# Kernel optimization log

Hardware: AMD Instinct MI355X
Metric: run time of the kernel (lower is better)

Reference implementation:

```python
import jax, jax.numpy as jnp
import numpy as np

B, N, H, A = 8, 2048, 512, 128


def setup_inputs() -> dict:
    key = jax.random.key(0)
    ks = jax.random.split(key, 7)
    s_h = 1.0 / np.sqrt(H)
    s_a = 1.0 / np.sqrt(A)
    return {
        "x": jax.random.normal(ks[0], (B, N, H), dtype=jnp.float32),
        "Wq": jax.random.uniform(ks[1], (H, A), jnp.float32, -s_h, s_h),
        "bq": jax.random.uniform(ks[2], (A,), jnp.float32, -s_h, s_h),
        "Wk": jax.random.uniform(ks[3], (H, A), jnp.float32, -s_h, s_h),
        "bk": jax.random.uniform(ks[4], (A,), jnp.float32, -s_h, s_h),
        "Wv": jax.random.uniform(ks[5], (A, 1), jnp.float32, -s_a, s_a),
        "bv": jax.random.uniform(ks[6], (1,), jnp.float32, -s_a, s_a),
    }


def reference(x, Wq, bq, Wk, bk, Wv, bv):
    # x: [B, N, H]
    Qw = x @ Wq + bq              # [B, N, A]
    Kw = x @ Wk + bk              # [B, N, A]
    g = jax.nn.sigmoid((Qw @ Wv + bv)[..., 0])  # [B, N] per-token gate

    n = x.shape[1]
    scores = jnp.einsum("bnd,bmd->bnm", Qw, Kw)  # [B, N, N]
    diag = jnp.eye(n, dtype=bool)
    # M adds -inf on the diagonal (ones + -inf = -inf), 0 elsewhere
    scores = jnp.where(diag, -jnp.inf, scores)
    P = jax.nn.softmax(scores, axis=-1)          # diagonal prob is exactly 0

    # D + (I - D) @ P with D = diag_embed(g) reduces to a per-row scale:
    # row i -> (1 - g_i) * P[i, :] plus g_i on the diagonal (P[i,i] == 0).
    eye = jnp.eye(n, dtype=P.dtype)
    out = (1.0 - g)[..., None] * P + eye * g[..., None]
    return out
```

## Files before the change

kernel.cpp:

```cpp
#include <hip/hip_runtime.h>
#include <hip/hip_bf16.h>
#include <math.h>

constexpr int B = 8, N = 2048, H = 512, A = 128;

typedef _Float16 f16x8 __attribute__((ext_vector_type(8)));
typedef float f32x4 __attribute__((ext_vector_type(4)));
typedef unsigned short ushort_t;
typedef unsigned int uint_t;

__device__ __forceinline__ f32x4 mfma16h(f16x8 a, f16x8 b, f32x4 c) {
    return __builtin_amdgcn_mfma_f32_16x16x32_f16(a, b, c, 0, 0, 0);
}
__device__ __forceinline__ ushort_t f2h(float v) {
    return __builtin_bit_cast(ushort_t, (_Float16)v);
}
__device__ __forceinline__ float h2f(ushort_t u) {
    return (float)__builtin_bit_cast(_Float16, u);
}
__device__ __forceinline__ void gload16(const void* g, void* l) {
    __builtin_amdgcn_global_load_lds(
        (__attribute__((address_space(1))) void*)(g),
        (__attribute__((address_space(3))) void*)(l), 16, 0, 0);
}
__device__ __forceinline__ int swz_byte(int rl, int col) {
    return (rl << 8) + ((((col >> 3) << 4) | ((col & 7) << 1)) ^ ((rl & 7) << 4));
}

__global__ __launch_bounds__(256) void k0_conv(
    const float* __restrict__ Wq, const float* __restrict__ Wk,
    ushort_t* __restrict__ WqT, ushort_t* __restrict__ WkT)
{
    const int id = blockIdx.x * 256 + threadIdx.x;
    const int k = id >> 7, n = id & 127;
    WqT[n * 512 + k] = f2h(Wq[id]);
    WkT[n * 512 + k] = f2h(Wk[id]);
}

__global__ __launch_bounds__(256) void k1_mfma(
    const float* __restrict__ x,
    const ushort_t* __restrict__ WqT, const ushort_t* __restrict__ WkT,
    const float* __restrict__ bq, const float* __restrict__ bk,
    const float* __restrict__ Wv, const float* __restrict__ bv,
    ushort_t* __restrict__ QSh, ushort_t* __restrict__ KSh,
    float* __restrict__ gb)
{
    __shared__ ushort_t xh[32 * 256];
    __shared__ float gred[2][32];
    const int t = threadIdx.x;
    const int lane = t & 63, w = t >> 6;
    const int l15 = lane & 15, l4 = lane >> 4;
    const int m0 = blockIdx.x * 32;

    f32x4 acc[2][4];
    #pragma unroll
    for (int r = 0; r < 2; ++r)
        #pragma unroll
        for (int c = 0; c < 4; ++c) acc[r][c] = {0.f, 0.f, 0.f, 0.f};

    const ushort_t* WT = (w < 2) ? WqT : WkT;
    const int colbase = (w & 1) * 64;

    for (int ck = 0; ck < 2; ++ck) {
        __syncthreads();
        #pragma unroll
        for (int it = 0; it < 8; ++it) {
            const int idx = it * 256 + t;
            const int row = idx >> 6, c4 = idx & 63;
            const float4 v = *(const float4*)(x + (size_t)(m0 + row) * H + ck * 256 + c4 * 4);
            uint2 hh;
            hh.x = (uint_t)f2h(v.x) | ((uint_t)f2h(v.y) << 16);
            hh.y = (uint_t)f2h(v.z) | ((uint_t)f2h(v.w) << 16);
            const int base = row * 512 + ((((c4 >> 1) << 4)) ^ ((row & 7) << 4)) + (c4 & 1) * 8;
            *(uint2*)((char*)xh + base) = hh;
        }
        __syncthreads();

        #pragma unroll
        for (int ks = 0; ks < 8; ++ks) {
            f16x8 ah[2], bh[4];
            const int kb = ks * 64 + l4 * 16;
            #pragma unroll
            for (int rb = 0; rb < 2; ++rb) {
                const int row = rb * 16 + l15;
                ah[rb] = *(const f16x8*)((const char*)xh + row * 512 + (kb ^ ((row & 7) << 4)));
            }
            const int kg = ck * 256 + ks * 32 + l4 * 8;
            #pragma unroll
            for (int cb = 0; cb < 4; ++cb)
                bh[cb] = *(const f16x8*)(WT + (size_t)(colbase + cb * 16 + l15) * 512 + kg);
            #pragma unroll
            for (int rb = 0; rb < 2; ++rb)
                #pragma unroll
                for (int cb = 0; cb < 4; ++cb)
                    acc[rb][cb] = mfma16h(ah[rb], bh[cb], acc[rb][cb]);
        }
    }

    const float* bias = (w < 2) ? bq : bk;
    float bb[4], wv[4];
    #pragma unroll
    for (int cb = 0; cb < 4; ++cb) {
        bb[cb] = bias[colbase + cb * 16 + l15];
        wv[cb] = Wv[colbase + cb * 16 + l15];
    }
    float p[2][4];
    #pragma unroll
    for (int rb = 0; rb < 2; ++rb)
        #pragma unroll
        for (int g = 0; g < 4; ++g) {
            float ps = 0.f;
            #pragma unroll
            for (int cb = 0; cb < 4; ++cb) {
                const float v = acc[rb][cb][g] + bb[cb];
                acc[rb][cb][g] = v;
                ps = fmaf(v, wv[cb], ps);
            }
            p[rb][g] = ps;
        }

    ushort_t* OS = (w < 2) ? QSh : KSh;
    #pragma unroll
    for (int rb = 0; rb < 2; ++rb) {
        #pragma unroll
        for (int cb = 0; cb < 4; ++cb) {
            const int col = colbase + cb * 16 + l15;
            #pragma unroll
            for (int g = 0; g < 4; ++g) {
                const int r = m0 + rb * 16 + l4 * 4 + g;
                const size_t blkb = (size_t)(r >> 7) * 32768;
                const int byte = swz_byte(r & 127, col);
                *(ushort_t*)((char*)OS + blkb + byte) = f2h(acc[rb][cb][g]);
            }
        }
    }

    if (w < 2) {
        #pragma unroll
        for (int rb = 0; rb < 2; ++rb)
            #pragma unroll
            for (int g = 0; g < 4; ++g) {
                float v = p[rb][g];
                v += __shfl_xor(v, 1); v += __shfl_xor(v, 2);
                v += __shfl_xor(v, 4); v += __shfl_xor(v, 8);
                if (l15 == 0) gred[w][rb * 16 + l4 * 4 + g] = v;
            }
    }
    __syncthreads();
    if (t < 32) {
        const float z = gred[0][t] + gred[1][t] + bv[0];
        gb[m0 + t] = 1.f / (1.f + __expf(-z));
    }
}

__global__ __launch_bounds__(256) void k2s_mfma(
    const ushort_t* __restrict__ QSh, const ushort_t* __restrict__ KSh,
    float* __restrict__ lpart)
{
    __shared__ ushort_t qh[16384], kh[16384];
    const int t = threadIdx.x;
    const int lane = t & 63, wid = t >> 6;
    const int wr = wid >> 1, wc = wid & 1;
    const int l15 = lane & 15, l4 = lane >> 4;

    const int b    = blockIdx.x & 7;
    const int rest = blockIdx.x >> 3;
    const int jc   = rest >> 4;
    const int i0   = (rest & 15) << 7;

    {
        const int qblk = (b << 4) + (i0 >> 7);
        const char* sh = (const char*)(QSh + (size_t)qblk * 16384);
        const int base = wid * 8192;
        #pragma unroll
        for (int it = 0; it < 8; ++it) {
            const int o = base + it * 1024;
            gload16(sh + o + lane * 16, (char*)qh + o);
        }
    }

    float lsum[4] = {0.f, 0.f, 0.f, 0.f};

    for (int jt = 0; jt < 4; ++jt) {
        __syncthreads();
        {
            const int kblk = (b << 4) + (jc << 2) + jt;
            const char* sk = (const char*)(KSh + (size_t)kblk * 16384);
            const int base = wid * 8192;
            #pragma unroll
            for (int it = 0; it < 8; ++it) {
                const int o = base + it * 1024;
                gload16(sk + o + lane * 16, (char*)kh + o);
            }
        }
        __syncthreads();

        const int j0 = jc * 512 + jt * 128;
        f32x4 acc[4][4];
        #pragma unroll
        for (int r = 0; r < 4; ++r)
            #pragma unroll
            for (int c = 0; c < 4; ++c) acc[r][c] = {0.f, 0.f, 0.f, 0.f};

        #pragma unroll
        for (int ks = 0; ks < 4; ++ks) {
            const int kb = ks * 64 + l4 * 16;
            f16x8 ak[4], bq[4];
            #pragma unroll
            for (int r = 0; r < 4; ++r) {
                const int row = wr * 64 + r * 16 + l15;
                ak[r] = *(const f16x8*)((const char*)kh + (row << 8) + (kb ^ ((row & 7) << 4)));
            }
            #pragma unroll
            for (int c = 0; c < 4; ++c) {
                const int row = wc * 64 + c * 16 + l15;
                bq[c] = *(const f16x8*)((const char*)qh + (row << 8) + (kb ^ ((row & 7) << 4)));
            }
            #pragma unroll
            for (int r = 0; r < 4; ++r)
                #pragma unroll
                for (int c = 0; c < 4; ++c)
                    acc[r][c] = mfma16h(ak[r], bq[c], acc[r][c]);
        }

        #pragma unroll
        for (int r = 0; r < 4; ++r) {
            const int jb = j0 + wr * 64 + r * 16 + l4 * 4;
            #pragma unroll
            for (int c = 0; c < 4; ++c) {
                const int i = i0 + wc * 64 + c * 16 + l15;
                #pragma unroll
                for (int g = 0; g < 4; ++g) {
                    const float e = (jb + g == i) ? 0.f : __expf(acc[r][c][g]);
                    lsum[c] += e;
                }
            }
        }
    }
    __syncthreads();

    float* lred = (float*)kh;
    #pragma unroll
    for (int c = 0; c < 4; ++c) {
        float v = lsum[c];
        v += __shfl_xor(v, 16); v += __shfl_xor(v, 32);
        if (lane < 16) lred[wid * 64 + c * 16 + l15] = v;
    }
    __syncthreads();
    if (t < 128) {
        const int wcb = t >> 6, cl = t & 63;
        const float l = lred[wcb * 64 + cl] + lred[(2 + wcb) * 64 + cl];
        lpart[(size_t)jc * (B * N) + (size_t)b * N + i0 + t] = l;
    }
}

__global__ __launch_bounds__(256) void k2w_mfma(
    const ushort_t* __restrict__ QSh, const ushort_t* __restrict__ KSh,
    const float* __restrict__ gb, const float* __restrict__ lpart,
    float* __restrict__ out)
{
    __shared__ ushort_t qh[16384], kh[16384];
    __shared__ float scl_s[128], gvv_s[128];
    const int t = threadIdx.x;
    const int lane = t & 63, wid = t >> 6;
    const int wr = wid >> 1, wc = wid & 1;
    const int l15 = lane & 15, l4 = lane >> 4;

    const int b    = blockIdx.x & 7;
    const int rest = blockIdx.x >> 3;
    const int jc   = rest >> 4;
    const int i0   = (rest & 15) << 7;
    const size_t BN = (size_t)B * N;
    const size_t bN = (size_t)b * N;

    if (t < 128) {
        const size_t row = bN + i0 + t;
        const float l = lpart[row] + lpart[BN + row] + lpart[2*BN + row] + lpart[3*BN + row];
        const float g = gb[row];
        scl_s[t] = (1.f - g) / l;
        gvv_s[t] = g;
    }

    {
        const int qblk = (b << 4) + (i0 >> 7);
        const char* sh = (const char*)(QSh + (size_t)qblk * 16384);
        const int base = wid * 8192;
        #pragma unroll
        for (int it = 0; it < 8; ++it) {
            const int o = base + it * 1024;
            gload16(sh + o + lane * 16, (char*)qh + o);
        }
    }

    for (int jt = 0; jt < 4; ++jt) {
        __syncthreads();
        {
            const int kblk = (b << 4) + (jc << 2) + jt;
            const char* sk = (const char*)(KSh + (size_t)kblk * 16384);
            const int base = wid * 8192;
            #pragma unroll
            for (int it = 0; it < 8; ++it) {
                const int o = base + it * 1024;
                gload16(sk + o + lane * 16, (char*)kh + o);
            }
        }
        __syncthreads();

        const int j0 = jc * 512 + jt * 128;
        f32x4 acc[4][4];
        #pragma unroll
        for (int r = 0; r < 4; ++r)
            #pragma unroll
            for (int c = 0; c < 4; ++c) acc[r][c] = {0.f, 0.f, 0.f, 0.f};

        #pragma unroll
        for (int ks = 0; ks < 4; ++ks) {
            const int kb = ks * 64 + l4 * 16;
            f16x8 ak[4], bq[4];
            #pragma unroll
            for (int r = 0; r < 4; ++r) {
                const int row = wr * 64 + r * 16 + l15;
                ak[r] = *(const f16x8*)((const char*)kh + (row << 8) + (kb ^ ((row & 7) << 4)));
            }
            #pragma unroll
            for (int c = 0; c < 4; ++c) {
                const int row = wc * 64 + c * 16 + l15;
                bq[c] = *(const f16x8*)((const char*)qh + (row << 8) + (kb ^ ((row & 7) << 4)));
            }
            #pragma unroll
            for (int r = 0; r < 4; ++r)
                #pragma unroll
                for (int c = 0; c < 4; ++c)
                    acc[r][c] = mfma16h(ak[r], bq[c], acc[r][c]);
        }

        #pragma unroll
        for (int r = 0; r < 4; ++r) {
            const int jb = j0 + wr * 64 + r * 16 + l4 * 4;
            #pragma unroll
            for (int c = 0; c < 4; ++c) {
                const int li = wc * 64 + c * 16 + l15;
                const int i = i0 + li;
                const float sc = scl_s[li], gv = gvv_s[li];
                float4 o;
                o.x = (jb + 0 == i) ? gv : __expf(acc[r][c][0]) * sc;
                o.y = (jb + 1 == i) ? gv : __expf(acc[r][c][1]) * sc;
                o.z = (jb + 2 == i) ? gv : __expf(acc[r][c][2]) * sc;
                o.w = (jb + 3 == i) ? gv : __expf(acc[r][c][3]) * sc;
                *(float4*)(out + (bN + i) * N + jb) = o;
            }
        }
    }
}

extern "C" void kernel_launch(void* const* d_in, const int* in_sizes, int n_in,
                              void* d_out, int out_size, void* d_ws, size_t ws_size,
                              hipStream_t stream) {
    const float* x  = (const float*)d_in[0];
    const float* Wq = (const float*)d_in[1];
    const float* bq = (const float*)d_in[2];
    const float* Wk = (const float*)d_in[3];
    const float* bk = (const float*)d_in[4];
    const float* Wv = (const float*)d_in[5];
    const float* bv = (const float*)d_in[6];
    float* out = (float*)d_out;

    const size_t PL = (size_t)B * N * A;
    ushort_t* QSh = (ushort_t*)d_ws;
    ushort_t* KSh = QSh + PL;
    ushort_t* WqT = KSh + PL;
    ushort_t* WkT = WqT + H * A;
    float* gb = (float*)(WkT + H * A);
    float* lp = gb + (size_t)B * N;

    k0_conv<<<(H * A) / 256, 256, 0, stream>>>(Wq, Wk, WqT, WkT);
    k1_mfma<<<(B * N) / 32, 256, 0, stream>>>(x, WqT, WkT, bq, bk, Wv, bv,
                                              QSh, KSh, gb);
    k2s_mfma<<<512, 256, 0, stream>>>(QSh, KSh, lp);
    k2w_mfma<<<512, 256, 0, stream>>>(QSh, KSh, gb, lp, out);
}
```

Baseline: 79.65 us.

## Keep Q fragments in registers and double-buffer K tiles in both score kernels

Both score kernels now load the Q tile's MFMA fragments into registers once, which frees its LDS buffer. The two LDS buffers then act as a ping-pong buffer for K tiles, so the next K tile is fetched while the current one is used for MFMA and exp. This removes the per-iteration barrier-then-load stall and repeated Q LDS reads. It costs more registers (a 4x4 array of f16x8 for Q), and launch_bounds now asks for 2 blocks per CU.

```diff
diff --git a/kernel.cpp b/kernel.cpp
--- a/kernel.cpp
+++ b/kernel.cpp
@@ -153,11 +153,11 @@
     }
 }
 
-__global__ __launch_bounds__(256) void k2s_mfma(
+__global__ __launch_bounds__(256, 2) void k2s_mfma(
     const ushort_t* __restrict__ QSh, const ushort_t* __restrict__ KSh,
     float* __restrict__ lpart)
 {
-    __shared__ ushort_t qh[16384], kh[16384];
+    __shared__ ushort_t ldsA[16384], ldsB[16384];
     const int t = threadIdx.x;
     const int lane = t & 63, wid = t >> 6;
     const int wr = wid >> 1, wc = wid & 1;
@@ -167,60 +167,70 @@
     const int rest = blockIdx.x >> 3;
     const int jc   = rest >> 4;
     const int i0   = (rest & 15) << 7;
+    const int base = wid * 8192;
+    const int kblk0 = (b << 4) + (jc << 2);
+
+    #define STAGE_K(jt, dst)                                                    \
+    {                                                                           \
+        const char* sk_ = (const char*)(KSh + (size_t)(kblk0 + (jt)) * 16384);  \
+        _Pragma("unroll")                                                       \
+        for (int it_ = 0; it_ < 8; ++it_) {                                     \
+            const int o_ = base + it_ * 1024;                                   \
+            gload16(sk_ + o_ + lane * 16, (char*)(dst) + o_);                   \
+        }                                                                       \
+    }
 
     {
         const int qblk = (b << 4) + (i0 >> 7);
-        const char* sh = (const char*)(QSh + (size_t)qblk * 16384);
-        const int base = wid * 8192;
+        const char* sq = (const char*)(QSh + (size_t)qblk * 16384);
         #pragma unroll
         for (int it = 0; it < 8; ++it) {
             const int o = base + it * 1024;
-            gload16(sh + o + lane * 16, (char*)qh + o);
-        }
-    }
-
-    float lsum[4] = {0.f, 0.f, 0.f, 0.f};
-
-    for (int jt = 0; jt < 4; ++jt) {
-        __syncthreads();
-        {
-            const int kblk = (b << 4) + (jc << 2) + jt;
-            const char* sk = (const char*)(KSh + (size_t)kblk * 16384);
-            const int base = wid * 8192;
-            #pragma unroll
-            for (int it = 0; it < 8; ++it) {
-                const int o = base + it * 1024;
-                gload16(sk + o + lane * 16, (char*)kh + o);
-            }
-        }
-        __syncthreads();
-
-        const int j0 = jc * 512 + jt * 128;
-        f32x4 acc[4][4];
-        #pragma unroll
-        for (int r = 0; r < 4; ++r)
-            #pragma unroll
-            for (int c = 0; c < 4; ++c) acc[r][c] = {0.f, 0.f, 0.f, 0.f};
-
+            gload16(sq + o + lane * 16, (char*)ldsA + o);
+        }
+        STAGE_K(0, ldsB);
+    }
+    __syncthreads();
+
+    f16x8 qreg[4][4];
+    #pragma unroll
+    for (int c = 0; c < 4; ++c) {
+        const int row = wc * 64 + c * 16 + l15;
         #pragma unroll
         for (int ks = 0; ks < 4; ++ks) {
             const int kb = ks * 64 + l4 * 16;
-            f16x8 ak[4], bq[4];
+            qreg[c][ks] = *(const f16x8*)((const char*)ldsA + (row << 8) + (kb ^ ((row & 7) << 4)));
+        }
+    }
+    __syncthreads();
+    STAGE_K(1, ldsA);
+
+    float lsum[4] = {0.f, 0.f, 0.f, 0.f};
+
+    for (int jt = 0; jt < 4; ++jt) {
+        const char* cur = (jt & 1) ? (const char*)ldsA : (const char*)ldsB;
+        const int j0 = jc * 512 + jt * 128;
+
+        f32x4 acc[4][4];
+        #pragma unroll
+        for (int r = 0; r < 4; ++r)
+            #pragma unroll
+            for (int c = 0; c < 4; ++c) acc[r][c] = {0.f, 0.f, 0.f, 0.f};
+
+        #pragma unroll
+        for (int ks = 0; ks < 4; ++ks) {
+            const int kb = ks * 64 + l4 * 16;
+            f16x8 ak[4];
             #pragma unroll
             for (int r = 0; r < 4; ++r) {
                 const int row = wr * 64 + r * 16 + l15;
-                ak[r] = *(const f16x8*)((const char*)kh + (row << 8) + (kb ^ ((row & 7) << 4)));
-            }
-            #pragma unroll
-            for (int c = 0; c < 4; ++c) {
-                const int row = wc * 64 + c * 16 + l15;
-                bq[c] = *(const f16x8*)((const char*)qh + (row << 8) + (kb ^ ((row & 7) << 4)));
+                ak[r] = *(const f16x8*)(cur + (row << 8) + (kb ^ ((row & 7) << 4)));
             }
             #pragma unroll
             for (int r = 0; r < 4; ++r)
                 #pragma unroll
                 for (int c = 0; c < 4; ++c)
-                    acc[r][c] = mfma16h(ak[r], bq[c], acc[r][c]);
+                    acc[r][c] = mfma16h(ak[r], qreg[c][ks], acc[r][c]);
         }
 
         #pragma unroll
@@ -236,10 +246,11 @@
                 }
             }
         }
-    }
-    __syncthreads();
-
-    float* lred = (float*)kh;
+        __syncthreads();
+        if (jt < 2) STAGE_K(jt + 2, (jt & 1) ? ldsA : ldsB);
+    }
+
+    float* lred = (float*)ldsB;
     #pragma unroll
     for (int c = 0; c < 4; ++c) {
         float v = lsum[c];
@@ -252,14 +263,15 @@
         const float l = lred[wcb * 64 + cl] + lred[(2 + wcb) * 64 + cl];
         lpart[(size_t)jc * (B * N) + (size_t)b * N + i0 + t] = l;
     }
-}
-
-__global__ __launch_bounds__(256) void k2w_mfma(
+    #undef STAGE_K
+}
+
+__global__ __launch_bounds__(256, 2) void k2w_mfma(
     const ushort_t* __restrict__ QSh, const ushort_t* __restrict__ KSh,
     const float* __restrict__ gb, const float* __restrict__ lpart,
     float* __restrict__ out)
 {
-    __shared__ ushort_t qh[16384], kh[16384];
+    __shared__ ushort_t ldsA[16384], ldsB[16384];
     __shared__ float scl_s[128], gvv_s[128];
     const int t = threadIdx.x;
     const int lane = t & 63, wid = t >> 6;
@@ -272,7 +284,29 @@
     const int i0   = (rest & 15) << 7;
     const size_t BN = (size_t)B * N;
     const size_t bN = (size_t)b * N;
-
+    const int base = wid * 8192;
+    const int kblk0 = (b << 4) + (jc << 2);
+
+    #define STAGE_K(jt, dst)                                                    \
+    {                                                                           \
+        const char* sk_ = (const char*)(KSh + (size_t)(kblk0 + (jt)) * 16384);  \
+        _Pragma("unroll")                                                       \
+        for (int it_ = 0; it_ < 8; ++it_) {                                     \
+            const int o_ = base + it_ * 1024;                                   \
+            gload16(sk_ + o_ + lane * 16, (char*)(dst) + o_);                   \
+        }                                                                       \
+    }
+
+    {
+        const int qblk = (b << 4) + (i0 >> 7);
+        const char* sq = (const char*)(QSh + (size_t)qblk * 16384);
+        #pragma unroll
+        for (int it = 0; it < 8; ++it) {
+            const int o = base + it * 1024;
+            gload16(sq + o + lane * 16, (char*)ldsA + o);
+        }
+        STAGE_K(0, ldsB);
+    }
     if (t < 128) {
         const size_t row = bN + i0 + t;
         const float l = lpart[row] + lpart[BN + row] + lpart[2*BN + row] + lpart[3*BN + row];
@@ -280,58 +314,45 @@
         scl_s[t] = (1.f - g) / l;
         gvv_s[t] = g;
     }
-
-    {
-        const int qblk = (b << 4) + (i0 >> 7);
-        const char* sh = (const char*)(QSh + (size_t)qblk * 16384);
-        const int base = wid * 8192;
-        #pragma unroll
-        for (int it = 0; it < 8; ++it) {
-            const int o = base + it * 1024;
-            gload16(sh + o + lane * 16, (char*)qh + o);
-        }
-    }
-
-    for (int jt = 0; jt < 4; ++jt) {
-        __syncthreads();
-        {
-            const int kblk = (b << 4) + (jc << 2) + jt;
-            const char* sk = (const char*)(KSh + (size_t)kblk * 16384);
-            const int base = wid * 8192;
-            #pragma unroll
-            for (int it = 0; it < 8; ++it) {
-                const int o = base + it * 1024;
-                gload16(sk + o + lane * 16, (char*)kh + o);
-            }
-        }
-        __syncthreads();
-
-        const int j0 = jc * 512 + jt * 128;
-        f32x4 acc[4][4];
-        #pragma unroll
-        for (int r = 0; r < 4; ++r)
-            #pragma unroll
-            for (int c = 0; c < 4; ++c) acc[r][c] = {0.f, 0.f, 0.f, 0.f};
-
+    __syncthreads();
+
+    f16x8 qreg[4][4];
+    #pragma unroll
+    for (int c = 0; c < 4; ++c) {
+        const int row = wc * 64 + c * 16 + l15;
         #pragma unroll
         for (int ks = 0; ks < 4; ++ks) {
             const int kb = ks * 64 + l4 * 16;
-            f16x8 ak[4], bq[4];
+            qreg[c][ks] = *(const f16x8*)((const char*)ldsA + (row << 8) + (kb ^ ((row & 7) << 4)));
+        }
+    }
+    __syncthreads();
+    STAGE_K(1, ldsA);
+
+    for (int jt = 0; jt < 4; ++jt) {
+        const char* cur = (jt & 1) ? (const char*)ldsA : (const char*)ldsB;
+        const int j0 = jc * 512 + jt * 128;
+
+        f32x4 acc[4][4];
+        #pragma unroll
+        for (int r = 0; r < 4; ++r)
+            #pragma unroll
+            for (int c = 0; c < 4; ++c) acc[r][c] = {0.f, 0.f, 0.f, 0.f};
+
+        #pragma unroll
+        for (int ks = 0; ks < 4; ++ks) {
+            const int kb = ks * 64 + l4 * 16;
+            f16x8 ak[4];
             #pragma unroll
             for (int r = 0; r < 4; ++r) {
                 const int row = wr * 64 + r * 16 + l15;
-                ak[r] = *(const f16x8*)((const char*)kh + (row << 8) + (kb ^ ((row & 7) << 4)));
-            }
-            #pragma unroll
-            for (int c = 0; c < 4; ++c) {
-                const int row = wc * 64 + c * 16 + l15;
-                bq[c] = *(const f16x8*)((const char*)qh + (row << 8) + (kb ^ ((row & 7) << 4)));
+                ak[r] = *(const f16x8*)(cur + (row << 8) + (kb ^ ((row & 7) << 4)));
             }
             #pragma unroll
             for (int r = 0; r < 4; ++r)
                 #pragma unroll
                 for (int c = 0; c < 4; ++c)
-                    acc[r][c] = mfma16h(ak[r], bq[c], acc[r][c]);
+                    acc[r][c] = mfma16h(ak[r], qreg[c][ks], acc[r][c]);
         }
 
         #pragma unroll
@@ -350,7 +371,10 @@
                 *(float4*)(out + (bN + i) * N + jb) = o;
             }
         }
-    }
+        __syncthreads();
+        if (jt < 2) STAGE_K(jt + 2, (jt & 1) ? ldsA : ldsB);
+    }
+    #undef STAGE_K
 }
 
 extern "C" void kernel_launch(void* const* d_in, const int* in_sizes, int n_in,
```

Measured after the change: 70.81 us. -11.1%, faster.
